# Performance work log

Hardware: AMD Instinct MI355X
Metric: run time of the kernel (lower is better)

## Reference

```python
import jax, jax.numpy as jnp
import numpy as np

B, K, F, E = 32, 1024, 128, 128  # batch, window_size(num_nodes), n_features, embed_dim
OUT2 = 125                       # lin2 output dim (hardcoded in module)
ALPHA = 0.2                      # LeakyReLU negative slope


def setup_inputs() -> dict:
    key = jax.random.key(0)
    ks = jax.random.split(key, 7)
    x = jax.random.normal(ks[0], (B, K, F), dtype=jnp.float32)
    lin_w = jax.random.normal(ks[1], (E, F), dtype=jnp.float32) * 0.05
    lin_b = jax.random.normal(ks[2], (E,), dtype=jnp.float32) * 0.01
    a = jax.random.normal(ks[3], (2 * E, 1), dtype=jnp.float32) * 0.1  # xavier-ish
    bias = jax.random.normal(ks[4], (K, K), dtype=jnp.float32) * 0.02
    lin2_w = jax.random.normal(ks[5], (OUT2, K), dtype=jnp.float32) * 0.03
    lin2_b = jax.random.normal(ks[6], (OUT2,), dtype=jnp.float32) * 0.01
    return {"x": x, "lin_w": lin_w, "lin_b": lin_b, "a": a, "bias": bias,
            "lin2_w": lin2_w, "lin2_b": lin2_b}


def reference(x, lin_w, lin_b, a, bias, lin2_w, lin2_b):
    # Wx = lin(x): [B,K,E]
    Wx = jnp.einsum('bkf,ef->bke', x, lin_w) + lin_b
    # Additive attention scores. Original concatenates (Wx_i, Wx_j) -> [B,K,K,2E]
    # then matmuls with a [2E,1]. Identity: concat @ a == Wx_i@a1 + Wx_j@a2.
    a1 = a[:E, 0]   # [E]
    a2 = a[E:, 0]   # [E]
    s1 = Wx @ a1    # [B,K]  (row/query term, from repeat_interleave)
    s2 = Wx @ a2    # [B,K]  (col/key term, from repeat)
    e = jax.nn.leaky_relu(s1[:, :, None] + s2[:, None, :], negative_slope=ALPHA)
    e = e + bias                              # [B,K,K]
    attention = jax.nn.softmax(e, axis=2)     # softmax over last dim (keys)
    h = jnp.einsum('bij,bjf->bif', attention, x) + x   # [B,K,F], residual
    # permute(0,2,1) -> [B,F,K]; lin2 contracts K -> 125
    h2 = jnp.einsum('bkf,ok->bfo', h, lin2_w) + lin2_b  # [B,F,125]
    h2 = jax.nn.relu(h2)
    return (h2, attention)
```

## Files before the change

kernel.cpp:

```cpp
#include <hip/hip_runtime.h>

#define B_ 32
#define K_ 1024
#define F_ 128
#define E_ 128
#define OUT2_ 125
#define ALPHA_ 0.2f

typedef __bf16 bf16x8_t __attribute__((ext_vector_type(8)));
typedef float  f32x4_t  __attribute__((ext_vector_type(4)));

__global__ __launch_bounds__(256) void k_xts(const float* __restrict__ x,
                                             const float* __restrict__ lin_w,
                                             const float* __restrict__ lin_b,
                                             const float* __restrict__ a,
                                             unsigned short* __restrict__ xt,
                                             float* __restrict__ s1,
                                             float* __restrict__ s2) {
    int kt = blockIdx.x;
    int b  = blockIdx.y;
    int t  = threadIdx.x;
    __shared__ float xs[64 * 132];
    __shared__ float red1[4][64], red2[4][64];
    __shared__ float wsl[260];

    {
        int f = t & 127, sel = t >> 7;
        const float* av = a + sel * 128;
        float acc = 0.f;
#pragma unroll 8
        for (int e = 0; e < E_; ++e) acc += lin_w[e * F_ + f] * av[e];
        wsl[sel * 128 + f] = acc;
        if (t < 2) {
            const float* aw = a + t * 128;
            float c = 0.f;
#pragma unroll 8
            for (int e = 0; e < E_; ++e) c += lin_b[e] * aw[e];
            wsl[256 + t] = c;
        }
    }
    const float* xb = x + ((size_t)b * K_ + kt * 64) * F_;
#pragma unroll
    for (int q = 0; q < 8; ++q) {
        int flat = q * 256 + t;
        int kk = flat >> 5, f4 = flat & 31;
        float4 v = *(const float4*)(xb + (size_t)kk * F_ + f4 * 4);
        xs[kk * 132 + f4 * 4]     = v.x;
        xs[kk * 132 + f4 * 4 + 1] = v.y;
        xs[kk * 132 + f4 * 4 + 2] = v.z;
        xs[kk * 132 + f4 * 4 + 3] = v.w;
    }
    __syncthreads();
    {
        int f = t >> 1, half = t & 1;
        union { __bf16 h[32]; uint4 v[4]; } pack;
#pragma unroll
        for (int i = 0; i < 32; ++i) pack.h[i] = (__bf16)xs[(half * 32 + i) * 132 + f];
        unsigned short* dst = xt + (((size_t)(b * 16 + kt) * 128 + f) * 64 + half * 32);
        uint4* d4 = (uint4*)dst;
#pragma unroll
        for (int i = 0; i < 4; ++i) d4[i] = pack.v[i];
    }
    {
        int r = t & 63, p = t >> 6;
        const float4* xr = (const float4*)&xs[r * 132 + p * 32];
        const float4* w1 = (const float4*)&wsl[p * 32];
        const float4* w2 = (const float4*)&wsl[128 + p * 32];
        float a1 = 0.f, a2 = 0.f;
#pragma unroll
        for (int q = 0; q < 8; ++q) {
            float4 xv = xr[q];
            float4 wa = w1[q], wb = w2[q];
            a1 += xv.x * wa.x + xv.y * wa.y + xv.z * wa.z + xv.w * wa.w;
            a2 += xv.x * wb.x + xv.y * wb.y + xv.z * wb.z + xv.w * wb.w;
        }
        red1[p][r] = a1; red2[p][r] = a2;
    }
    __syncthreads();
    if (t < 64) {
        s1[(size_t)b * K_ + kt * 64 + t] =
            red1[0][t] + red1[1][t] + red1[2][t] + red1[3][t] + wsl[256];
    } else if (t < 128) {
        int r = t - 64;
        s2[(size_t)b * K_ + kt * 64 + r] =
            red2[0][r] + red2[1][r] + red2[2][r] + red2[3][r] + wsl[257];
    }
}

__global__ __launch_bounds__(256) void k_softmax(const float* __restrict__ s1,
                                                 const float* __restrict__ s2,
                                                 const float* __restrict__ bias,
                                                 float* __restrict__ att) {
    int i = blockIdx.x >> 5;
    int b = blockIdx.x & 31;
    int t = threadIdx.x;
    float sv = s1[b * K_ + i];
    float4 s2v = ((const float4*)(s2 + b * K_))[t];
    float4 bv  = ((const float4*)(bias + (size_t)i * K_))[t];
    float e[4];
    {
        float v;
        v = sv + s2v.x; v = v > 0.f ? v : ALPHA_ * v; e[0] = __expf(v + bv.x);
        v = sv + s2v.y; v = v > 0.f ? v : ALPHA_ * v; e[1] = __expf(v + bv.y);
        v = sv + s2v.z; v = v > 0.f ? v : ALPHA_ * v; e[2] = __expf(v + bv.z);
        v = sv + s2v.w; v = v > 0.f ? v : ALPHA_ * v; e[3] = __expf(v + bv.w);
    }
    float sum = e[0] + e[1] + e[2] + e[3];
    for (int m = 32; m; m >>= 1) sum += __shfl_xor(sum, m, 64);
    __shared__ float reds[4];
    int wave = t >> 6, lane = t & 63;
    if (lane == 0) reds[wave] = sum;
    __syncthreads();
    sum = reds[0] + reds[1] + reds[2] + reds[3];
    float r = 1.f / sum;
    float4 o; o.x = e[0] * r; o.y = e[1] * r; o.z = e[2] * r; o.w = e[3] * r;
    ((float4*)(att + ((size_t)b * K_ + i) * K_))[t] = o;
}

__global__ __launch_bounds__(256, 8) void k_attx(const float* __restrict__ att,
                                                 const unsigned short* __restrict__ xt,
                                                 const float* __restrict__ x,
                                                 unsigned short* __restrict__ ht) {
    int flatb = blockIdx.y * gridDim.x + blockIdx.x;
    int swz   = (flatb & 7) * 128 + (flatb >> 3);
    int b  = swz >> 5;
    int i0 = (swz & 31) * 32;
    int t  = threadIdx.x;
    int wave = t >> 6, lane = t & 63;
    int quad = lane >> 4, l15 = lane & 15;

    __shared__ unsigned short A_s[2][32 * 64];

    int ar = t >> 3, ag = t & 7;
    const float* asrc = att + ((size_t)b * K_ + i0 + ar) * K_ + ag * 8;
    const int aofs = ar * 64 + 8 * (ag ^ (ar & 7));

    const unsigned short* xb = xt + (size_t)b * 16 * 128 * 64
                             + ((size_t)(wave * 32 + l15)) * 64 + quad * 8;

    f32x4_t acc[2][2];
#pragma unroll
    for (int m = 0; m < 2; ++m)
#pragma unroll
        for (int n = 0; n < 2; ++n) acc[m][n] = (f32x4_t)(0.f);

    {
        float4 a0 = *(const float4*)(asrc);
        float4 a1 = *(const float4*)(asrc + 4);
        union { __bf16 h[8]; uint4 v; } p;
        p.h[0] = (__bf16)a0.x; p.h[1] = (__bf16)a0.y;
        p.h[2] = (__bf16)a0.z; p.h[3] = (__bf16)a0.w;
        p.h[4] = (__bf16)a1.x; p.h[5] = (__bf16)a1.y;
        p.h[6] = (__bf16)a1.z; p.h[7] = (__bf16)a1.w;
        *(uint4*)&A_s[0][aofs] = p.v;
    }
    __syncthreads();

#pragma unroll 2
    for (int kt = 0; kt < 16; ++kt) {
        int cur = kt & 1;
        const unsigned short* xk = xb + (size_t)kt * 128 * 64;
        float4 an0, an1;
        if (kt < 15) {
            const float* as2 = asrc + (kt + 1) * 64;
            an0 = *(const float4*)(as2);
            an1 = *(const float4*)(as2 + 4);
        }
        bf16x8_t bff[2][2];
#pragma unroll
        for (int kh = 0; kh < 2; ++kh) {
            bff[kh][0] = *(const bf16x8_t*)(xk + kh * 32);
            bff[kh][1] = *(const bf16x8_t*)(xk + 16 * 64 + kh * 32);
        }
#pragma unroll
        for (int kh = 0; kh < 2; ++kh) {
            int g = (kh << 2) | quad;
            bf16x8_t af[2];
#pragma unroll
            for (int m = 0; m < 2; ++m) {
                int row = m * 16 + l15;
                af[m] = *(const bf16x8_t*)&A_s[cur][row * 64 + 8 * (g ^ (row & 7))];
            }
#pragma unroll
            for (int m = 0; m < 2; ++m)
#pragma unroll
                for (int n = 0; n < 2; ++n)
                    acc[m][n] = __builtin_amdgcn_mfma_f32_16x16x32_bf16(af[m], bff[kh][n], acc[m][n], 0, 0, 0);
        }
        if (kt < 15) {
            union { __bf16 h[8]; uint4 v; } p;
            p.h[0] = (__bf16)an0.x; p.h[1] = (__bf16)an0.y;
            p.h[2] = (__bf16)an0.z; p.h[3] = (__bf16)an0.w;
            p.h[4] = (__bf16)an1.x; p.h[5] = (__bf16)an1.y;
            p.h[6] = (__bf16)an1.z; p.h[7] = (__bf16)an1.w;
            *(uint4*)&A_s[cur ^ 1][aofs] = p.v;
        }
        __syncthreads();
    }
#pragma unroll
    for (int m = 0; m < 2; ++m) {
#pragma unroll
        for (int n = 0; n < 2; ++n) {
            int f = wave * 32 + n * 16 + l15;
            int ib = i0 + m * 16 + quad * 4;
            union { __bf16 h[4]; ushort4 v; } p;
#pragma unroll
            for (int r = 0; r < 4; ++r) {
                int i = ib + r;
                p.h[r] = (__bf16)(acc[m][n][r] + x[((size_t)b * K_ + i) * F_ + f]);
            }
            *(ushort4*)&ht[((size_t)b * F_ + f) * K_ + ib] = p.v;
        }
    }
}

__global__ __launch_bounds__(256) void k_out2m(const unsigned short* __restrict__ ht,
                                               const float* __restrict__ w2,
                                               float* __restrict__ part) {
    int b  = blockIdx.y;
    int f0 = blockIdx.x * 64;
    int ks = blockIdx.z;
    int t  = threadIdx.x;
    int wave = t >> 6, lane = t & 63;
    int quad = lane >> 4, l15 = lane & 15;

    __shared__ unsigned short W_s[128 * 72];
    __shared__ unsigned short H_s[64 * 72];

    f32x4_t acc[8];
#pragma unroll
    for (int m = 0; m < 8; ++m) acc[m] = (f32x4_t)(0.f);

    int wo = t >> 1, wq = t & 1;
    int hf = t >> 2, hq = t & 3;

    int kt0 = ks * 4;
    for (int kt = kt0; kt < kt0 + 4; ++kt) {
        int k0 = kt * 64;
        __syncthreads();
        {
            union { __bf16 h[32]; uint4 v[4]; } p;
            if (wo < OUT2_) {
                const float* src = w2 + (size_t)wo * K_ + k0 + wq * 32;
#pragma unroll
                for (int q = 0; q < 8; ++q) {
                    float4 v = *(const float4*)(src + q * 4);
                    p.h[q * 4]     = (__bf16)v.x;
                    p.h[q * 4 + 1] = (__bf16)v.y;
                    p.h[q * 4 + 2] = (__bf16)v.z;
                    p.h[q * 4 + 3] = (__bf16)v.w;
                }
            } else {
#pragma unroll
                for (int q = 0; q < 4; ++q) p.v[q] = make_uint4(0, 0, 0, 0);
            }
            uint4* d = (uint4*)&W_s[wo * 72 + wq * 32];
#pragma unroll
            for (int q = 0; q < 4; ++q) d[q] = p.v[q];
        }
        {
            const uint4* src = (const uint4*)(ht + ((size_t)b * F_ + f0 + hf) * K_ + k0) + hq * 2;
            uint4* d = (uint4*)&H_s[hf * 72 + hq * 16];
            d[0] = src[0]; d[1] = src[1];
        }
        __syncthreads();
#pragma unroll
        for (int kh = 0; kh < 2; ++kh) {
            bf16x8_t bf = *(const bf16x8_t*)&H_s[(wave * 16 + l15) * 72 + kh * 32 + quad * 8];
#pragma unroll
            for (int m = 0; m < 8; ++m) {
                bf16x8_t af = *(const bf16x8_t*)&W_s[(m * 16 + l15) * 72 + kh * 32 + quad * 8];
                acc[m] = __builtin_amdgcn_mfma_f32_16x16x32_bf16(af, bf, acc[m], 0, 0, 0);
            }
        }
    }
    int f = f0 + wave * 16 + l15;
    float* prow = part + ((size_t)(ks * 32 + b) * 128 + f) * 128;
#pragma unroll
    for (int m = 0; m < 8; ++m)
        *(f32x4_t*)&prow[m * 16 + quad * 4] = acc[m];
}

__global__ __launch_bounds__(256) void k_out2e(const float* __restrict__ part,
                                               const float* __restrict__ b2,
                                               float* __restrict__ out) {
    int idx = blockIdx.x * 256 + threadIdx.x;
    if (idx >= B_ * F_ * OUT2_) return;
    int o  = idx % OUT2_;
    int bf = idx / OUT2_;
    float v = b2[o];
#pragma unroll
    for (int s = 0; s < 4; ++s) v += part[((size_t)s * 4096 + bf) * 128 + o];
    out[idx] = v > 0.f ? v : 0.f;
}

extern "C" void kernel_launch(void* const* d_in, const int* in_sizes, int n_in,
                              void* d_out, int out_size, void* d_ws, size_t ws_size,
                              hipStream_t stream) {
    const float* x      = (const float*)d_in[0];
    const float* lin_w  = (const float*)d_in[1];
    const float* lin_b  = (const float*)d_in[2];
    const float* a      = (const float*)d_in[3];
    const float* bias   = (const float*)d_in[4];
    const float* lin2_w = (const float*)d_in[5];
    const float* lin2_b = (const float*)d_in[6];

    float* out = (float*)d_out;
    float* h2  = out;
    float* att = out + (size_t)B_ * F_ * OUT2_;

    float* ws = (float*)d_ws;
    float* s1 = ws + 512;
    float* s2 = ws + 512 + B_ * K_;
    unsigned short* ht = (unsigned short*)(ws + 512 + 2 * B_ * K_);
    unsigned short* xt = ht + (size_t)B_ * K_ * F_;
    float* part = (float*)xt;

    k_xts<<<dim3(16, B_), 256, 0, stream>>>(x, lin_w, lin_b, a, xt, s1, s2);
    k_softmax<<<B_ * K_, 256, 0, stream>>>(s1, s2, bias, att);
    k_attx<<<dim3(K_ / 32, B_), 256, 0, stream>>>(att, xt, x, ht);
    k_out2m<<<dim3(2, B_, 4), 256, 0, stream>>>(ht, lin2_w, part);
    k_out2e<<<(B_ * F_ * OUT2_ + 255) / 256, 256, 0, stream>>>(part, lin2_b, h2);
}
```

Baseline: 250.3 us.

## Fuse lin2 split-K kernels into one epilogue kernel and stream attention loads

Replaces the split-K lin2 GEMM plus separate reduction/bias/ReLU kernel with a single kernel that tiles 16 features per block, loops over all of K, and applies bias and ReLU directly. This removes the partial-sum buffer traffic and one kernel launch. In exchange, each block re-converts the whole lin2 weight matrix to bf16, which adds redundant weight loads. Separately, attention reads in the att@x kernel become nontemporal loads so the streamed attention matrix does not pollute the cache.

```diff
diff --git a/kernel.cpp b/kernel.cpp
--- a/kernel.cpp
+++ b/kernel.cpp
@@ -145,13 +145,13 @@
         for (int n = 0; n < 2; ++n) acc[m][n] = (f32x4_t)(0.f);
 
     {
-        float4 a0 = *(const float4*)(asrc);
-        float4 a1 = *(const float4*)(asrc + 4);
+        f32x4_t a0 = __builtin_nontemporal_load((const f32x4_t*)(asrc));
+        f32x4_t a1 = __builtin_nontemporal_load((const f32x4_t*)(asrc + 4));
         union { __bf16 h[8]; uint4 v; } p;
-        p.h[0] = (__bf16)a0.x; p.h[1] = (__bf16)a0.y;
-        p.h[2] = (__bf16)a0.z; p.h[3] = (__bf16)a0.w;
-        p.h[4] = (__bf16)a1.x; p.h[5] = (__bf16)a1.y;
-        p.h[6] = (__bf16)a1.z; p.h[7] = (__bf16)a1.w;
+        p.h[0] = (__bf16)a0[0]; p.h[1] = (__bf16)a0[1];
+        p.h[2] = (__bf16)a0[2]; p.h[3] = (__bf16)a0[3];
+        p.h[4] = (__bf16)a1[0]; p.h[5] = (__bf16)a1[1];
+        p.h[6] = (__bf16)a1[2]; p.h[7] = (__bf16)a1[3];
         *(uint4*)&A_s[0][aofs] = p.v;
     }
     __syncthreads();
@@ -160,11 +160,11 @@
     for (int kt = 0; kt < 16; ++kt) {
         int cur = kt & 1;
         const unsigned short* xk = xb + (size_t)kt * 128 * 64;
-        float4 an0, an1;
+        f32x4_t an0, an1;
         if (kt < 15) {
             const float* as2 = asrc + (kt + 1) * 64;
-            an0 = *(const float4*)(as2);
-            an1 = *(const float4*)(as2 + 4);
+            an0 = __builtin_nontemporal_load((const f32x4_t*)(as2));
+            an1 = __builtin_nontemporal_load((const f32x4_t*)(as2 + 4));
         }
         bf16x8_t bff[2][2];
 #pragma unroll
@@ -189,10 +189,10 @@
         }
         if (kt < 15) {
             union { __bf16 h[8]; uint4 v; } p;
-            p.h[0] = (__bf16)an0.x; p.h[1] = (__bf16)an0.y;
-            p.h[2] = (__bf16)an0.z; p.h[3] = (__bf16)an0.w;
-            p.h[4] = (__bf16)an1.x; p.h[5] = (__bf16)an1.y;
-            p.h[6] = (__bf16)an1.z; p.h[7] = (__bf16)an1.w;
+            p.h[0] = (__bf16)an0[0]; p.h[1] = (__bf16)an0[1];
+            p.h[2] = (__bf16)an0[2]; p.h[3] = (__bf16)an0[3];
+            p.h[4] = (__bf16)an1[0]; p.h[5] = (__bf16)an1[1];
+            p.h[6] = (__bf16)an1[2]; p.h[7] = (__bf16)an1[3];
             *(uint4*)&A_s[cur ^ 1][aofs] = p.v;
         }
         __syncthreads();
@@ -214,28 +214,27 @@
     }
 }
 
-__global__ __launch_bounds__(256) void k_out2m(const unsigned short* __restrict__ ht,
-                                               const float* __restrict__ w2,
-                                               float* __restrict__ part) {
+__global__ __launch_bounds__(256) void k_out2(const unsigned short* __restrict__ ht,
+                                              const float* __restrict__ w2,
+                                              const float* __restrict__ b2,
+                                              float* __restrict__ out) {
     int b  = blockIdx.y;
-    int f0 = blockIdx.x * 64;
-    int ks = blockIdx.z;
+    int f0 = blockIdx.x * 16;
     int t  = threadIdx.x;
     int wave = t >> 6, lane = t & 63;
     int quad = lane >> 4, l15 = lane & 15;
 
     __shared__ unsigned short W_s[128 * 72];
-    __shared__ unsigned short H_s[64 * 72];
-
-    f32x4_t acc[8];
-#pragma unroll
-    for (int m = 0; m < 8; ++m) acc[m] = (f32x4_t)(0.f);
+    __shared__ unsigned short H_s[16 * 72];
+
+    f32x4_t acc[2];
+    acc[0] = (f32x4_t)(0.f);
+    acc[1] = (f32x4_t)(0.f);
 
     int wo = t >> 1, wq = t & 1;
-    int hf = t >> 2, hq = t & 3;
-
-    int kt0 = ks * 4;
-    for (int kt = kt0; kt < kt0 + 4; ++kt) {
+    int hf = t >> 3, hq = t & 7;
+
+    for (int kt = 0; kt < 16; ++kt) {
         int k0 = kt * 64;
         __syncthreads();
         {
@@ -258,40 +257,36 @@
 #pragma unroll
             for (int q = 0; q < 4; ++q) d[q] = p.v[q];
         }
-        {
-            const uint4* src = (const uint4*)(ht + ((size_t)b * F_ + f0 + hf) * K_ + k0) + hq * 2;
-            uint4* d = (uint4*)&H_s[hf * 72 + hq * 16];
-            d[0] = src[0]; d[1] = src[1];
+        if (t < 128) {
+            *(uint4*)&H_s[hf * 72 + hq * 8] =
+                *(const uint4*)(ht + ((size_t)b * F_ + f0 + hf) * K_ + k0 + hq * 8);
         }
         __syncthreads();
 #pragma unroll
         for (int kh = 0; kh < 2; ++kh) {
-            bf16x8_t bf = *(const bf16x8_t*)&H_s[(wave * 16 + l15) * 72 + kh * 32 + quad * 8];
-#pragma unroll
-            for (int m = 0; m < 8; ++m) {
+            bf16x8_t bf = *(const bf16x8_t*)&H_s[l15 * 72 + kh * 32 + quad * 8];
+#pragma unroll
+            for (int j = 0; j < 2; ++j) {
+                int m = wave * 2 + j;
                 bf16x8_t af = *(const bf16x8_t*)&W_s[(m * 16 + l15) * 72 + kh * 32 + quad * 8];
-                acc[m] = __builtin_amdgcn_mfma_f32_16x16x32_bf16(af, bf, acc[m], 0, 0, 0);
-            }
-        }
-    }
-    int f = f0 + wave * 16 + l15;
-    float* prow = part + ((size_t)(ks * 32 + b) * 128 + f) * 128;
-#pragma unroll
-    for (int m = 0; m < 8; ++m)
-        *(f32x4_t*)&prow[m * 16 + quad * 4] = acc[m];
-}
-
-__global__ __launch_bounds__(256) void k_out2e(const float* __restrict__ part,
-                                               const float* __restrict__ b2,
-                                               float* __restrict__ out) {
-    int idx = blockIdx.x * 256 + threadIdx.x;
-    if (idx >= B_ * F_ * OUT2_) return;
-    int o  = idx % OUT2_;
-    int bf = idx / OUT2_;
-    float v = b2[o];
-#pragma unroll
-    for (int s = 0; s < 4; ++s) v += part[((size_t)s * 4096 + bf) * 128 + o];
-    out[idx] = v > 0.f ? v : 0.f;
+                acc[j] = __builtin_amdgcn_mfma_f32_16x16x32_bf16(af, bf, acc[j], 0, 0, 0);
+            }
+        }
+    }
+    int f = f0 + l15;
+    float* orow = out + ((size_t)b * F_ + f) * OUT2_;
+#pragma unroll
+    for (int j = 0; j < 2; ++j) {
+        int ob = (wave * 2 + j) * 16 + quad * 4;
+#pragma unroll
+        for (int r = 0; r < 4; ++r) {
+            int o = ob + r;
+            if (o < OUT2_) {
+                float v = acc[j][r] + b2[o];
+                orow[o] = v > 0.f ? v : 0.f;
+            }
+        }
+    }
 }
 
 extern "C" void kernel_launch(void* const* d_in, const int* in_sizes, int n_in,
@@ -314,11 +309,9 @@
     float* s2 = ws + 512 + B_ * K_;
     unsigned short* ht = (unsigned short*)(ws + 512 + 2 * B_ * K_);
     unsigned short* xt = ht + (size_t)B_ * K_ * F_;
-    float* part = (float*)xt;
 
     k_xts<<<dim3(16, B_), 256, 0, stream>>>(x, lin_w, lin_b, a, xt, s1, s2);
     k_softmax<<<B_ * K_, 256, 0, stream>>>(s1, s2, bias, att);
     k_attx<<<dim3(K_ / 32, B_), 256, 0, stream>>>(att, xt, x, ht);
-    k_out2m<<<dim3(2, B_, 4), 256, 0, stream>>>(ht, lin2_w, part);
-    k_out2e<<<(B_ * F_ * OUT2_ + 255) / 256, 256, 0, stream>>>(part, lin2_b, h2);
-}
+    k_out2<<<dim3(F_ / 16, B_), 256, 0, stream>>>(ht, lin2_w, lin2_b, h2);
+}
```

Measured after the change: 294.6 us. 1.18x slower.
